# Optimization experiments

Measured on AMD Instinct MI355X. Metric: run time of the kernel, lower is better.

## Reference

```python
import jax, jax.numpy as jnp
import numpy as np

EMBED_DIM = 768
NUM_HEADS = 12
HEAD_DIM = EMBED_DIM // NUM_HEADS
SCALE = HEAD_DIM ** -0.5


def setup_inputs() -> dict:
    key = jax.random.key(0)
    ks = jax.random.split(key, 9)
    B, S, D = 2, 2048, EMBED_DIM
    init = 1.0 / np.sqrt(D)  # ~ nn.Linear default uniform scale
    x = jax.random.normal(ks[0], (B, S, D), dtype=jnp.float32)
    Wq = jax.random.uniform(ks[1], (D, D), jnp.float32, -init, init)
    bq = jax.random.uniform(ks[2], (D,), jnp.float32, -init, init)
    Wk = jax.random.uniform(ks[3], (D, D), jnp.float32, -init, init)
    bk = jax.random.uniform(ks[4], (D,), jnp.float32, -init, init)
    Wv = jax.random.uniform(ks[5], (D, D), jnp.float32, -init, init)
    bv = jax.random.uniform(ks[6], (D,), jnp.float32, -init, init)
    Wo = jax.random.uniform(ks[7], (D, D), jnp.float32, -init, init)
    bo = jax.random.uniform(ks[8], (D,), jnp.float32, -init, init)
    return {"x": x, "Wq": Wq, "bq": bq, "Wk": Wk, "bk": bk,
            "Wv": Wv, "bv": bv, "Wo": Wo, "bo": bo}


def reference(x, Wq, bq, Wk, bk, Wv, bv, Wo, bo):
    B, S, D = x.shape
    H, Dh = NUM_HEADS, HEAD_DIM
    # projections; weights stored as (in, out) so x @ W == torch Linear with W.T
    q = (x @ Wq + bq).reshape(B, S, H, Dh).transpose(0, 2, 1, 3)  # [B,H,S,Dh]
    k = (x @ Wk + bk).reshape(B, S, H, Dh).transpose(0, 2, 1, 3)
    v = (x @ Wv + bv).reshape(B, S, H, Dh).transpose(0, 2, 1, 3)
    scores = jnp.einsum("bhqd,bhkd->bhqk", q, k) * SCALE        # [B,H,S,S]
    weights = jax.nn.softmax(scores, axis=-1)
    out = jnp.einsum("bhqk,bhkd->bhqd", weights, v)              # [B,H,S,Dh]
    out = out.transpose(0, 2, 1, 3).reshape(B, S, D)
    return out @ Wo + bo
```

## Files before the change

### kernel.cpp

```cpp
#include <hip/hip_runtime.h>
#include <math.h>

#define BB 2
#define SS 2048
#define DDIM 768
#define HH 12
#define DH 64
#define NROWS (BB*SS)
#define NTOK_D (NROWS*DDIM)
#define NQT2 (SS/128)

typedef _Float16 f16;
typedef _Float16 half4 __attribute__((ext_vector_type(4)));
typedef _Float16 half8 __attribute__((ext_vector_type(8)));
typedef float f32x4 __attribute__((ext_vector_type(4)));

#define MFMA16(a,b,c) __builtin_amdgcn_mfma_f32_16x16x32_f16((a),(b),(c),0,0,0)
#define QSCALE (0.125f * 1.44269504088896f)
#define DEFER_THR 8.0f

__device__ __forceinline__ int swz(int row, int chunk16) {
    return row*128 + ((chunk16 ^ (row & 7)) << 4);
}

__global__ __launch_bounds__(256) void prep_x(const float* __restrict__ x, f16* __restrict__ xh)
{
    int i = blockIdx.x * 256 + threadIdx.x;
    const float4* in = (const float4*)x;
    float4 a = in[i*2], b = in[i*2+1];
    half8 h = {(f16)a.x,(f16)a.y,(f16)a.z,(f16)a.w,(f16)b.x,(f16)b.y,(f16)b.z,(f16)b.w};
    *(half8*)(xh + (size_t)i*8) = h;
}

__global__ __launch_bounds__(256) void prep_w(const float* __restrict__ Wq, const float* __restrict__ Wk,
                                              const float* __restrict__ Wv, const float* __restrict__ Wo,
                                              f16* __restrict__ Wt)
{
    const int z = blockIdx.z;
    const float* W = z==0 ? Wq : (z==1 ? Wk : (z==2 ? Wv : Wo));
    f16* out = Wt + (size_t)z * DDIM * DDIM;

    __shared__ float tile[64][65];
    const int t = threadIdx.x;
    const int k0 = blockIdx.x*64, n0 = blockIdx.y*64;

    const int kr = t >> 2, nc = (t & 3) * 16;
    #pragma unroll
    for (int i = 0; i < 4; ++i) {
        float4 v = *(const float4*)&W[(size_t)(k0+kr)*DDIM + n0 + nc + i*4];
        tile[kr][nc+i*4+0] = v.x; tile[kr][nc+i*4+1] = v.y;
        tile[kr][nc+i*4+2] = v.z; tile[kr][nc+i*4+3] = v.w;
    }
    __syncthreads();
    const int nr = t >> 2, kc = (t & 3) * 16;
    half8 h0, h1;
    #pragma unroll
    for (int j = 0; j < 8; ++j) {
        h0[j] = (f16)tile[kc + j][nr];
        h1[j] = (f16)tile[kc + 8 + j][nr];
    }
    *(half8*)&out[(size_t)(n0+nr)*DDIM + k0 + kc]     = h0;
    *(half8*)&out[(size_t)(n0+nr)*DDIM + k0 + kc + 8] = h1;
}

__global__ __launch_bounds__(256) void proj_qkv(const f16* __restrict__ Xh, const f16* __restrict__ Wt,
        const float* __restrict__ bq, const float* __restrict__ bk, const float* __restrict__ bv,
        f16* __restrict__ qb, f16* __restrict__ kb2, f16* __restrict__ vtb)
{
    const int z = blockIdx.z;
    const f16* Wz = Wt + (size_t)z * DDIM * DDIM;
    const float* bias = z==0 ? bq : (z==1 ? bk : bv);
    const float qscale = (z==0) ? QSCALE : 1.0f;

    __shared__ __align__(16) unsigned char lds[24*1024];
    unsigned char* As = lds;
    unsigned char* Bs = lds + 8*1024;

    const int tid = threadIdx.x;
    const int l = tid & 63, w = tid >> 6;
    const int wm = w >> 1, wn = w & 1;
    const int m0 = blockIdx.x * 64, n0 = blockIdx.y * 128;

    f32x4 acc[2][4];
    #pragma unroll
    for (int i=0;i<2;i++)
        #pragma unroll
        for (int j=0;j<4;j++) { f32x4 zv = {0.f,0.f,0.f,0.f}; acc[i][j] = zv; }

    for (int k0 = 0; k0 < DDIM; k0 += 64) {
        __syncthreads();
        #pragma unroll
        for (int i = 0; i < 2; ++i) {
            int c = tid + i*256;
            int row = c >> 3, kc = c & 7;
            half8 v = *(const half8*)&Xh[(size_t)(m0+row)*DDIM + k0 + kc*8];
            *(half8*)(As + swz(row, kc)) = v;
        }
        #pragma unroll
        for (int i = 0; i < 4; ++i) {
            int c = tid + i*256;
            int row = c >> 3, kc = c & 7;
            half8 v = *(const half8*)&Wz[(size_t)(n0+row)*DDIM + k0 + kc*8];
            *(half8*)(Bs + swz(row, kc)) = v;
        }
        __syncthreads();

        half8 af[2][2], bf[4][2];
        #pragma unroll
        for (int mt = 0; mt < 2; ++mt) {
            int row = wm*32 + mt*16 + (l & 15);
            #pragma unroll
            for (int kh = 0; kh < 2; ++kh)
                af[mt][kh] = *(const half8*)(As + swz(row, kh*4 + (l>>4)));
        }
        #pragma unroll
        for (int nt = 0; nt < 4; ++nt) {
            int row = wn*64 + nt*16 + (l & 15);
            #pragma unroll
            for (int kh = 0; kh < 2; ++kh)
                bf[nt][kh] = *(const half8*)(Bs + swz(row, kh*4 + (l>>4)));
        }
        #pragma unroll
        for (int mt = 0; mt < 2; ++mt)
            #pragma unroll
            for (int nt = 0; nt < 4; ++nt) {
                acc[mt][nt] = MFMA16(af[mt][0], bf[nt][0], acc[mt][nt]);
                acc[mt][nt] = MFMA16(af[mt][1], bf[nt][1], acc[mt][nt]);
            }
    }

    if (z == 2) {
        #pragma unroll
        for (int mt = 0; mt < 2; ++mt)
            #pragma unroll
            for (int nt = 0; nt < 4; ++nt) {
                int m = m0 + wm*32 + mt*16 + (l>>4)*4;
                int n = n0 + wn*64 + nt*16 + (l & 15);
                int b = m >> 11, s = m & 2047;
                int h = n >> 6,  d = n & 63;
                float bs = bias[n];
                half4 o4 = {(f16)(acc[mt][nt][0] + bs), (f16)(acc[mt][nt][1] + bs),
                            (f16)(acc[mt][nt][2] + bs), (f16)(acc[mt][nt][3] + bs)};
                *(half4*)&vtb[(((size_t)(b*HH + h))*DH + d)*SS + s] = o4;
            }
    } else {
        f16* out = (z == 0) ? qb : kb2;
        #pragma unroll
        for (int mt = 0; mt < 2; ++mt)
            #pragma unroll
            for (int nt = 0; nt < 4; ++nt)
                #pragma unroll
                for (int r = 0; r < 4; ++r) {
                    int m = m0 + wm*32 + mt*16 + (l>>4)*4 + r;
                    int n = n0 + wn*64 + nt*16 + (l & 15);
                    float v = (acc[mt][nt][r] + bias[n]) * qscale;
                    int b = m >> 11, s = m & 2047;
                    int h = n >> 6,  d = n & 63;
                    out[(((size_t)(b*HH + h))*SS + s)*DH + d] = (f16)v;
                }
    }
}

__global__ __launch_bounds__(256) void attn_mfma(
        const f16* __restrict__ qbuf, const f16* __restrict__ kbuf,
        const f16* __restrict__ vtbuf, f16* __restrict__ pO, float2* __restrict__ mlb)
{
    __shared__ __align__(16) unsigned char lds[32*1024];

    const int tid = threadIdx.x;
    const int l = tid & 63, w = tid >> 6;
    const int g = l >> 4, qi = l & 15;
    const int qt = blockIdx.x, h = blockIdx.y;
    const int b = blockIdx.z >> 1, khalf = blockIdx.z & 1;
    const int q0 = qt * 128 + w * 32;
    const size_t base = ((size_t)(b * HH + h)) * SS * DH;
    const int key0 = khalf * (SS/2);
    const int pid = (b * HH + h) * NQT2 + qt;

    unsigned char* Kb = lds;
    unsigned char* Vb = lds + 8192;
    unsigned char* Pw = lds + 16384 + w*4096;

    half8 qf[2][2];
    #pragma unroll
    for (int f = 0; f < 2; ++f)
        #pragma unroll
        for (int kh = 0; kh < 2; ++kh)
            qf[f][kh] = *(const half8*)&qbuf[base + (size_t)(q0 + f*16 + qi)*DH + kh*32 + g*8];

    f32x4 oacc[2][4];
    #pragma unroll
    for (int f = 0; f < 2; ++f)
        #pragma unroll
        for (int i = 0; i < 4; ++i) { f32x4 zv = {0.f,0.f,0.f,0.f}; oacc[f][i] = zv; }
    float mrun[2] = {-INFINITY, -INFINITY};
    float lsum[2] = {0.f, 0.f};

    half8 sk[2], svv[2];

#define LOADT(t) { \
        _Pragma("unroll") \
        for (int i = 0; i < 2; ++i) { \
            int c = i*256 + tid, row = c >> 3, col = c & 7; \
            sk[i]  = *(const half8*)&kbuf[base + (size_t)(key0 + (t)*64 + row)*DH + col*8]; \
            svv[i] = *(const half8*)&vtbuf[base + (size_t)row*SS + key0 + (t)*64 + col*8]; \
        } }

#define WRT { \
        _Pragma("unroll") \
        for (int i = 0; i < 2; ++i) { \
            int c = i*256 + tid, row = c >> 3, col = c & 7; \
            *(half8*)(Kb + swz(row, col)) = sk[i]; \
            *(half8*)(Vb + swz(row, col)) = svv[i]; \
        } }

    LOADT(0); WRT;
    __syncthreads();

    for (int t = 0; t < 16; ++t) {
        if (t < 15) LOADT(t+1);

        half8 kf[8];
        #pragma unroll
        for (int mt = 0; mt < 4; ++mt)
            #pragma unroll
            for (int kh = 0; kh < 2; ++kh)
                kf[mt*2+kh] = *(const half8*)(Kb + swz(mt*16 + qi, kh*4 + g));
        half8 vf[8];
        #pragma unroll
        for (int dt = 0; dt < 4; ++dt)
            #pragma unroll
            for (int kh = 0; kh < 2; ++kh)
                vf[dt*2+kh] = *(const half8*)(Vb + swz(dt*16 + qi, kh*4 + g));

        #pragma unroll
        for (int f = 0; f < 2; ++f) {
            f32x4 sv[4];
            __builtin_amdgcn_s_setprio(1);
            #pragma unroll
            for (int mt = 0; mt < 4; ++mt) {
                f32x4 zz = {0.f,0.f,0.f,0.f};
                zz = MFMA16(kf[mt*2+0], qf[f][0], zz);
                sv[mt] = MFMA16(kf[mt*2+1], qf[f][1], zz);
            }
            __builtin_amdgcn_s_setprio(0);
            float lm = -INFINITY;
            #pragma unroll
            for (int mt = 0; mt < 4; ++mt)
                #pragma unroll
                for (int r = 0; r < 4; ++r) lm = fmaxf(lm, sv[mt][r]);
            lm = fmaxf(lm, __shfl_xor(lm, 16));
            lm = fmaxf(lm, __shfl_xor(lm, 32));
            if (!__all(lm <= mrun[f] + DEFER_THR)) {
                float mnew = fmaxf(mrun[f], lm);
                float fsc = exp2f(mrun[f] - mnew);
                mrun[f] = mnew;
                lsum[f] *= fsc;
                #pragma unroll
                for (int dt = 0; dt < 4; ++dt)
                    #pragma unroll
                    for (int r = 0; r < 4; ++r) oacc[f][dt][r] *= fsc;
            }
            float rs = 0.f;
            #pragma unroll
            for (int mt = 0; mt < 4; ++mt)
                #pragma unroll
                for (int r = 0; r < 4; ++r) {
                    float pv = exp2f(sv[mt][r] - mrun[f]);
                    sv[mt][r] = pv; rs += pv;
                }
            rs += __shfl_xor(rs, 16);
            rs += __shfl_xor(rs, 32);
            lsum[f] += rs;
            #pragma unroll
            for (int mt = 0; mt < 4; ++mt) {
                half4 pk = {(f16)sv[mt][0], (f16)sv[mt][1], (f16)sv[mt][2], (f16)sv[mt][3]};
                *(half4*)(Pw + swz(f*16 + qi, 2*mt + (g>>1)) + (g&1)*8) = pk;
            }
        }

        #pragma unroll
        for (int f = 0; f < 2; ++f) {
            half8 pf0 = *(const half8*)(Pw + swz(f*16 + qi, g));
            half8 pf1 = *(const half8*)(Pw + swz(f*16 + qi, 4 + g));
            __builtin_amdgcn_s_setprio(1);
            #pragma unroll
            for (int dt = 0; dt < 4; ++dt) {
                oacc[f][dt] = MFMA16(vf[dt*2+0], pf0, oacc[f][dt]);
                oacc[f][dt] = MFMA16(vf[dt*2+1], pf1, oacc[f][dt]);
            }
            __builtin_amdgcn_s_setprio(0);
        }

        if (t < 15) {
            __syncthreads();
            WRT;
            __syncthreads();
        }
    }

    f16* po = pO + ((size_t)pid*2 + khalf) * (128*64);
    float2* mlp = mlb + ((size_t)pid*2 + khalf) * 128;
    #pragma unroll
    for (int f = 0; f < 2; ++f) {
        const int qw = w*32 + f*16 + qi;
        const float inv = 1.0f / lsum[f];
        #pragma unroll
        for (int dt = 0; dt < 4; ++dt) {
            half4 o4 = {(f16)(oacc[f][dt][0]*inv), (f16)(oacc[f][dt][1]*inv),
                        (f16)(oacc[f][dt][2]*inv), (f16)(oacc[f][dt][3]*inv)};
            *(half4*)&po[qw*64 + dt*16 + g*4] = o4;
        }
        if (g == 0) mlp[qw] = make_float2(mrun[f], lsum[f]);
    }
#undef LOADT
#undef WRT
}

__global__ __launch_bounds__(256) void attn_combine(
        const f16* __restrict__ pO, const float2* __restrict__ mlb, f16* __restrict__ ob)
{
    const int gr = blockIdx.x*64 + (threadIdx.x >> 2);
    const int dg = (threadIdx.x & 3) << 4;
    const int bh = gr >> 11, s = gr & 2047;
    const int qt = s >> 7, qr = s & 127;
    const int pid = bh * NQT2 + qt;

    const f16* O0 = pO + ((size_t)pid*2 + 0)*(128*64) + qr*64;
    const f16* O1 = pO + ((size_t)pid*2 + 1)*(128*64) + qr*64;
    float2 a = mlb[((size_t)pid*2 + 0)*128 + qr];
    float2 c = mlb[((size_t)pid*2 + 1)*128 + qr];
    float M = fmaxf(a.x, c.x);
    float w0 = exp2f(a.x - M) * a.y;
    float w1 = exp2f(c.x - M) * c.y;
    float inv = 1.0f / (w0 + w1);
    w0 *= inv; w1 *= inv;

    half8 x0 = *(const half8*)&O0[dg];
    half8 x1 = *(const half8*)&O0[dg + 8];
    half8 y0 = *(const half8*)&O1[dg];
    half8 y1 = *(const half8*)&O1[dg + 8];
    half8 r0, r1;
    #pragma unroll
    for (int j = 0; j < 8; ++j) {
        r0[j] = (f16)(w0*(float)x0[j] + w1*(float)y0[j]);
        r1[j] = (f16)(w0*(float)x1[j] + w1*(float)y1[j]);
    }
    f16* dst = &ob[((size_t)bh*SS + s)*DH + dg];
    *(half8*)dst = r0;
    *(half8*)(dst + 8) = r1;
}

__global__ __launch_bounds__(256) void proj_out(const f16* __restrict__ obuf, const f16* __restrict__ Wt,
                                                const float* __restrict__ bo, float* __restrict__ out)
{
    const f16* Wz = Wt + (size_t)3 * DDIM * DDIM;

    __shared__ __align__(16) unsigned char lds[24*1024];
    unsigned char* As = lds;
    unsigned char* Bs = lds + 8*1024;

    const int tid = threadIdx.x;
    const int l = tid & 63, w = tid >> 6;
    const int wm = w >> 1, wn = w & 1;
    const int m0 = blockIdx.x * 64, n0 = blockIdx.y * 128;

    f32x4 acc[2][4];
    #pragma unroll
    for (int i=0;i<2;i++)
        #pragma unroll
        for (int j=0;j<4;j++) { f32x4 zv = {0.f,0.f,0.f,0.f}; acc[i][j] = zv; }

    for (int k0 = 0; k0 < DDIM; k0 += 64) {
        const int h = k0 >> 6;
        __syncthreads();
        #pragma unroll
        for (int i = 0; i < 2; ++i) {
            int c = tid + i*256;
            int row = c >> 3, kc = c & 7;
            int m = m0 + row, b = m >> 11, s = m & 2047;
            half8 v = *(const half8*)&obuf[(((size_t)(b*HH + h))*SS + s)*DH + kc*8];
            *(half8*)(As + swz(row, kc)) = v;
        }
        #pragma unroll
        for (int i = 0; i < 4; ++i) {
            int c = tid + i*256;
            int row = c >> 3, kc = c & 7;
            half8 v = *(const half8*)&Wz[(size_t)(n0+row)*DDIM + k0 + kc*8];
            *(half8*)(Bs + swz(row, kc)) = v;
        }
        __syncthreads();

        half8 af[2][2], bf[4][2];
        #pragma unroll
        for (int mt = 0; mt < 2; ++mt) {
            int row = wm*32 + mt*16 + (l & 15);
            #pragma unroll
            for (int kh = 0; kh < 2; ++kh)
                af[mt][kh] = *(const half8*)(As + swz(row, kh*4 + (l>>4)));
        }
        #pragma unroll
        for (int nt = 0; nt < 4; ++nt) {
            int row = wn*64 + nt*16 + (l & 15);
            #pragma unroll
            for (int kh = 0; kh < 2; ++kh)
                bf[nt][kh] = *(const half8*)(Bs + swz(row, kh*4 + (l>>4)));
        }
        #pragma unroll
        for (int mt = 0; mt < 2; ++mt)
            #pragma unroll
            for (int nt = 0; nt < 4; ++nt) {
                acc[mt][nt] = MFMA16(af[mt][0], bf[nt][0], acc[mt][nt]);
                acc[mt][nt] = MFMA16(af[mt][1], bf[nt][1], acc[mt][nt]);
            }
    }

    #pragma unroll
    for (int mt = 0; mt < 2; ++mt)
        #pragma unroll
        for (int nt = 0; nt < 4; ++nt)
            #pragma unroll
            for (int r = 0; r < 4; ++r) {
                int m = m0 + wm*32 + mt*16 + (l>>4)*4 + r;
                int n = n0 + wn*64 + nt*16 + (l & 15);
                out[(size_t)m*DDIM + n] = acc[mt][nt][r] + bo[n];
            }
}

extern "C" void kernel_launch(void* const* d_in, const int* in_sizes, int n_in,
                              void* d_out, int out_size, void* d_ws, size_t ws_size,
                              hipStream_t stream)
{
    const float* x  = (const float*)d_in[0];
    const float* Wq = (const float*)d_in[1];
    const float* bq = (const float*)d_in[2];
    const float* Wk = (const float*)d_in[3];
    const float* bk = (const float*)d_in[4];
    const float* Wv = (const float*)d_in[5];
    const float* bv = (const float*)d_in[6];
    const float* Wo = (const float*)d_in[7];
    const float* bo = (const float*)d_in[8];

    char* ws = (char*)d_ws;
    const size_t XH_B  = (size_t)NTOK_D * 2;
    const size_t WT_B  = (size_t)4 * DDIM * DDIM * 2;
    const size_t HB_B  = (size_t)BB * HH * SS * DH * 2;
    const size_t PO_B  = (size_t)BB * HH * NQT2 * 2 * 128 * 64 * 2;

    f16* Xh = (f16*)ws;
    f16* Wt = (f16*)(ws + XH_B);
    f16* qb = (f16*)(ws + XH_B + WT_B);
    f16* kb = (f16*)(ws + XH_B + WT_B + HB_B);
    f16* vt = (f16*)(ws + XH_B + WT_B + 2*HB_B);
    f16* ob = (f16*)(ws + XH_B + WT_B + 3*HB_B);
    f16* pO = (f16*)(ws + XH_B + WT_B + 4*HB_B);
    float2* mlb = (float2*)(ws + XH_B + WT_B + 4*HB_B + PO_B);

    prep_x<<<NTOK_D/(256*8), 256, 0, stream>>>(x, Xh);
    prep_w<<<dim3(DDIM/64, DDIM/64, 4), 256, 0, stream>>>(Wq, Wk, Wv, Wo, Wt);
    proj_qkv<<<dim3(NROWS/64, DDIM/128, 3), 256, 0, stream>>>(Xh, Wt, bq, bk, bv, qb, kb, vt);
    attn_mfma<<<dim3(NQT2, HH, BB*2), 256, 0, stream>>>(qb, kb, vt, pO, mlb);
    attn_combine<<<dim3(BB*HH*SS/64), 256, 0, stream>>>(pO, mlb, ob);
    proj_out<<<dim3(NROWS/64, DDIM/128), 256, 0, stream>>>(ob, Wt, bo, (float*)d_out);
}
```

Measured before the change: 125.4 us.

## Double-buffer K/V tiles in LDS and pack softmax exponentials to fp16

Splits the K/V shared-memory staging into two buffers so the next tile is written into the alternate buffer while the current one is consumed. This cuts the two barriers per iteration down to one. The softmax step now converts exponentials with packed round-toward-zero fp16 conversion, sums them in fp16 pairs, and uses a tree max reduction. LDS use rises from 32KB to 48KB per block, which may lower occupancy, and summing the row totals in fp16 costs some precision.

```diff
diff --git a/kernel.cpp b/kernel.cpp
--- a/kernel.cpp
+++ b/kernel.cpp
@@ -11,9 +11,16 @@
 #define NQT2 (SS/128)
 
 typedef _Float16 f16;
+typedef _Float16 half2v __attribute__((ext_vector_type(2)));
+typedef __fp16 fp16x2 __attribute__((ext_vector_type(2)));
 typedef _Float16 half4 __attribute__((ext_vector_type(4)));
 typedef _Float16 half8 __attribute__((ext_vector_type(8)));
 typedef float f32x4 __attribute__((ext_vector_type(4)));
+
+__device__ __forceinline__ half2v cvt_pk_f16(float a, float b) {
+    fp16x2 t = __builtin_amdgcn_cvt_pkrtz(a, b);
+    return __builtin_bit_cast(half2v, t);
+}
 
 #define MFMA16(a,b,c) __builtin_amdgcn_mfma_f32_16x16x32_f16((a),(b),(c),0,0,0)
 #define QSCALE (0.125f * 1.44269504088896f)
@@ -165,7 +172,7 @@
         const f16* __restrict__ qbuf, const f16* __restrict__ kbuf,
         const f16* __restrict__ vtbuf, f16* __restrict__ pO, float2* __restrict__ mlb)
 {
-    __shared__ __align__(16) unsigned char lds[32*1024];
+    __shared__ __align__(16) unsigned char lds[48*1024];
 
     const int tid = threadIdx.x;
     const int l = tid & 63, w = tid >> 6;
@@ -177,9 +184,7 @@
     const int key0 = khalf * (SS/2);
     const int pid = (b * HH + h) * NQT2 + qt;
 
-    unsigned char* Kb = lds;
-    unsigned char* Vb = lds + 8192;
-    unsigned char* Pw = lds + 16384 + w*4096;
+    unsigned char* Pw = lds + 32768 + w*4096;
 
     half8 qf[2][2];
     #pragma unroll
@@ -206,19 +211,25 @@
             svv[i] = *(const half8*)&vtbuf[base + (size_t)row*SS + key0 + (t)*64 + col*8]; \
         } }
 
-#define WRT { \
+#define WRT(bufi) { \
+        unsigned char* Kw_ = lds + (bufi)*16384; \
+        unsigned char* Vw_ = Kw_ + 8192; \
         _Pragma("unroll") \
         for (int i = 0; i < 2; ++i) { \
             int c = i*256 + tid, row = c >> 3, col = c & 7; \
-            *(half8*)(Kb + swz(row, col)) = sk[i]; \
-            *(half8*)(Vb + swz(row, col)) = svv[i]; \
+            *(half8*)(Kw_ + swz(row, col)) = sk[i]; \
+            *(half8*)(Vw_ + swz(row, col)) = svv[i]; \
         } }
 
-    LOADT(0); WRT;
+    LOADT(0); WRT(0);
     __syncthreads();
 
     for (int t = 0; t < 16; ++t) {
+        const int cur = t & 1;
         if (t < 15) LOADT(t+1);
+
+        const unsigned char* Kb = lds + cur*16384;
+        const unsigned char* Vb = Kb + 8192;
 
         half8 kf[8];
         #pragma unroll
@@ -244,11 +255,11 @@
                 sv[mt] = MFMA16(kf[mt*2+1], qf[f][1], zz);
             }
             __builtin_amdgcn_s_setprio(0);
-            float lm = -INFINITY;
-            #pragma unroll
-            for (int mt = 0; mt < 4; ++mt)
-                #pragma unroll
-                for (int r = 0; r < 4; ++r) lm = fmaxf(lm, sv[mt][r]);
+            float m0v = fmaxf(fmaxf(sv[0][0], sv[0][1]), fmaxf(sv[0][2], sv[0][3]));
+            float m1v = fmaxf(fmaxf(sv[1][0], sv[1][1]), fmaxf(sv[1][2], sv[1][3]));
+            float m2v = fmaxf(fmaxf(sv[2][0], sv[2][1]), fmaxf(sv[2][2], sv[2][3]));
+            float m3v = fmaxf(fmaxf(sv[3][0], sv[3][1]), fmaxf(sv[3][2], sv[3][3]));
+            float lm = fmaxf(fmaxf(m0v, m1v), fmaxf(m2v, m3v));
             lm = fmaxf(lm, __shfl_xor(lm, 16));
             lm = fmaxf(lm, __shfl_xor(lm, 32));
             if (!__all(lm <= mrun[f] + DEFER_THR)) {
@@ -261,22 +272,25 @@
                     #pragma unroll
                     for (int r = 0; r < 4; ++r) oacc[f][dt][r] *= fsc;
             }
-            float rs = 0.f;
-            #pragma unroll
-            for (int mt = 0; mt < 4; ++mt)
-                #pragma unroll
-                for (int r = 0; r < 4; ++r) {
-                    float pv = exp2f(sv[mt][r] - mrun[f]);
-                    sv[mt][r] = pv; rs += pv;
-                }
+            half2v ph[8];
+            #pragma unroll
+            for (int mt = 0; mt < 4; ++mt) {
+                float e0 = exp2f(sv[mt][0] - mrun[f]);
+                float e1 = exp2f(sv[mt][1] - mrun[f]);
+                float e2 = exp2f(sv[mt][2] - mrun[f]);
+                float e3 = exp2f(sv[mt][3] - mrun[f]);
+                ph[mt*2+0] = cvt_pk_f16(e0, e1);
+                ph[mt*2+1] = cvt_pk_f16(e2, e3);
+                half4 pk = {ph[mt*2+0][0], ph[mt*2+0][1], ph[mt*2+1][0], ph[mt*2+1][1]};
+                *(half4*)(Pw + swz(f*16 + qi, 2*mt + (g>>1)) + (g&1)*8) = pk;
+            }
+            half2v s01 = (ph[0] + ph[1]) + (ph[2] + ph[3]);
+            half2v s23 = (ph[4] + ph[5]) + (ph[6] + ph[7]);
+            half2v st = s01 + s23;
+            float rs = (float)st[0] + (float)st[1];
             rs += __shfl_xor(rs, 16);
             rs += __shfl_xor(rs, 32);
             lsum[f] += rs;
-            #pragma unroll
-            for (int mt = 0; mt < 4; ++mt) {
-                half4 pk = {(f16)sv[mt][0], (f16)sv[mt][1], (f16)sv[mt][2], (f16)sv[mt][3]};
-                *(half4*)(Pw + swz(f*16 + qi, 2*mt + (g>>1)) + (g&1)*8) = pk;
-            }
         }
 
         #pragma unroll
@@ -292,11 +306,8 @@
             __builtin_amdgcn_s_setprio(0);
         }
 
-        if (t < 15) {
-            __syncthreads();
-            WRT;
-            __syncthreads();
-        }
+        if (t < 15) WRT(cur^1);
+        __syncthreads();
     }
 
     f16* po = pO + ((size_t)pid*2 + khalf) * (128*64);
```

Result: no change. 125.0 us (-0.3%).
